# Performance work log

Hardware: AMD Instinct MI355X
Metric: run time of the kernel (lower is better)

The kernel has to match this reference:

```python
import math
import jax, jax.numpy as jnp
import numpy as np

L, B, S, D, H, F, V = 6, 2, 2048, 1024, 16, 4096, 32000
DK = D // H
EPS = 1e-5


def setup_inputs() -> dict:
    key = jax.random.key(0)
    ks = jax.random.split(key, 16)
    sc = 0.02
    inp = {
        "tokens": jax.random.randint(ks[0], (B, S), 0, V),
        "mask": jnp.ones((B, S), dtype=jnp.int32),
        "emb": jax.random.normal(ks[1], (V, D), jnp.float32) * sc,
        "Wq": jax.random.normal(ks[2], (L, D, D), jnp.float32) * sc,
        "bq": jnp.zeros((L, D), jnp.float32),
        "Wk": jax.random.normal(ks[3], (L, D, D), jnp.float32) * sc,
        "bk": jnp.zeros((L, D), jnp.float32),
        "Wv": jax.random.normal(ks[4], (L, D, D), jnp.float32) * sc,
        "bv": jnp.zeros((L, D), jnp.float32),
        "Wo": jax.random.normal(ks[5], (L, D, D), jnp.float32) * sc,
        "bo": jnp.zeros((L, D), jnp.float32),
        "W1": jax.random.normal(ks[6], (L, D, F), jnp.float32) * sc,
        "b1": jnp.zeros((L, F), jnp.float32),
        "W2": jax.random.normal(ks[7], (L, F, D), jnp.float32) * sc,
        "b2": jnp.zeros((L, D), jnp.float32),
        "g1": jnp.ones((L, D), jnp.float32),
        "be1": jnp.zeros((L, D), jnp.float32),
        "g2": jnp.ones((L, D), jnp.float32),
        "be2": jnp.zeros((L, D), jnp.float32),
        "gf": jnp.ones((D,), jnp.float32),
        "bf": jnp.zeros((D,), jnp.float32),
    }
    return inp


def _ln(x, g, b):
    m = jnp.mean(x, axis=-1, keepdims=True)
    v = jnp.var(x, axis=-1, keepdims=True)
    return (x - m) * jax.lax.rsqrt(v + EPS) * g + b


def _pos_encoding(seq_len, d_model, dtype):
    pos = jnp.arange(seq_len, dtype=jnp.float32)[:, None]
    div = jnp.exp(jnp.arange(0, d_model, 2, dtype=jnp.float32) * (-math.log(10000.0) / d_model))
    pe = jnp.zeros((seq_len, d_model), jnp.float32)
    pe = pe.at[:, 0::2].set(jnp.sin(pos * div)).at[:, 1::2].set(jnp.cos(pos * div))
    return pe.astype(dtype)


def reference(tokens, mask, emb, Wq, bq, Wk, bk, Wv, bv, Wo, bo,
              W1, b1, W2, b2, g1, be1, g2, be2, gf, bf):
    # NOTE: source scales embedding by sqrt(seq_len) (x.size(-1) of the TOKEN tensor)
    x = emb[tokens] * jnp.asarray(math.sqrt(S), emb.dtype)  # (B,S,D)
    x = x + _pos_encoding(S, D, x.dtype)[None]
    mbool = (mask == 0)[:, None, None, :]  # (B,1,1,S)
    inv_sqrt_dk = 1.0 / math.sqrt(DK)
    for i in range(L):
        h = _ln(x, g1[i], be1[i])
        q = (h @ Wq[i] + bq[i]).reshape(B, S, H, DK)
        k = (h @ Wk[i] + bk[i]).reshape(B, S, H, DK)
        v = (h @ Wv[i] + bv[i]).reshape(B, S, H, DK)
        scores = jnp.einsum('bqhd,bkhd->bhqk', q, k) * inv_sqrt_dk
        scores = jnp.where(mbool, jnp.asarray(-1e9, scores.dtype), scores)
        probs = jax.nn.softmax(scores, axis=-1)
        attn = jnp.einsum('bhqk,bkhd->bqhd', probs, v).reshape(B, S, D)
        x = x + (attn @ Wo[i] + bo[i])
        h2 = _ln(x, g2[i], be2[i])
        x = x + (jax.nn.relu(h2 @ W1[i] + b1[i]) @ W2[i] + b2[i])
    return _ln(x, gf, bf)
```

## Files before the change

### kernel.cpp

```cpp
#include <hip/hip_runtime.h>


typedef __bf16 bf16;
typedef __bf16 bf16x8 __attribute__((ext_vector_type(8)));
typedef __bf16 bf16x4 __attribute__((ext_vector_type(4)));
typedef float  f32x4  __attribute__((ext_vector_type(4)));

#define DEV __device__ __forceinline__

DEV float ld_raw(const void* p, size_t idx, int flag) {
  return flag ? (float)((const bf16*)p)[idx] : ((const float*)p)[idx];
}

DEV void gload16(const void* g, void* l) {
  __builtin_amdgcn_global_load_lds(
      (const __attribute__((address_space(1))) void*)g,
      (__attribute__((address_space(3))) void*)l, 16, 0, 0);
}

__global__ void k_sniff(const unsigned* g1, int* flag) {
  if (threadIdx.x == 0) *flag = (g1[0] == 0x3F803F80u) ? 1 : 0;
}

__global__ __launch_bounds__(256) void k_embed(
    const int* __restrict__ tokens, const void* __restrict__ emb,
    const int* __restrict__ flagp, float* __restrict__ x) {
  int row = blockIdx.x;
  int s = row & 2047;
  int flag = *flagp;
  int tok = tokens[row];
  int d0 = threadIdx.x * 4;
  float o[4];
#pragma unroll
  for (int c = 0; c < 4; ++c) {
    int d = d0 + c;
    float e = ld_raw(emb, (size_t)tok * 1024 + d, flag);
    int p2 = d & ~1;
    float div = expf((float)p2 * (-9.210340371976184f / 1024.0f));
    float arg = (float)s * div;
    float pe = (d & 1) ? cosf(arg) : sinf(arg);
    o[c] = e * 45.254833995939045f + pe;
  }
  float4 v = make_float4(o[0], o[1], o[2], o[3]);
  *(float4*)&x[(size_t)row * 1024 + d0] = v;
}

template <int OUTMODE>
__global__ __launch_bounds__(256) void k_ln(
    const float* __restrict__ x, const void* __restrict__ g,
    const void* __restrict__ b, int goff, const int* __restrict__ flagp,
    void* __restrict__ out) {
  int flag = *flagp;
  int row = blockIdx.x, t = threadIdx.x;
  float4 v = *(const float4*)&x[(size_t)row * 1024 + t * 4];
  float vv[4] = {v.x, v.y, v.z, v.w};
  float s = vv[0] + vv[1] + vv[2] + vv[3];
  float sq = vv[0]*vv[0] + vv[1]*vv[1] + vv[2]*vv[2] + vv[3]*vv[3];
#pragma unroll
  for (int off = 1; off < 64; off <<= 1) {
    s += __shfl_xor(s, off);
    sq += __shfl_xor(sq, off);
  }
  __shared__ float red[8];
  int w = t >> 6, l = t & 63;
  if (l == 0) { red[w * 2] = s; red[w * 2 + 1] = sq; }
  __syncthreads();
  s = red[0] + red[2] + red[4] + red[6];
  sq = red[1] + red[3] + red[5] + red[7];
  float mean = s * (1.0f / 1024.0f);
  float var = sq * (1.0f / 1024.0f) - mean * mean;
  float rstd = rsqrtf(var + 1e-5f);
#pragma unroll
  for (int c = 0; c < 4; ++c) {
    int d = t * 4 + c;
    float gv = ld_raw(g, (size_t)goff + d, flag);
    float bv = ld_raw(b, (size_t)goff + d, flag);
    float r = (vv[c] - mean) * rstd * gv + bv;
    size_t oi = (size_t)row * 1024 + d;
    if (OUTMODE == 0) {
      ((bf16*)out)[oi] = (bf16)r;
    } else {
      if (flag) ((unsigned short*)out)[oi] = __builtin_bit_cast(unsigned short, (bf16)r);
      else      ((float*)out)[oi] = r;
    }
  }
}

__global__ __launch_bounds__(256) void k_wtrans(
    const void* Wq, const void* Wk, const void* Wv, const void* Wo,
    const void* W1, const void* W2, int layer, const int* __restrict__ flagp,
    bf16* dQKV, bf16* dWo, bf16* dW1, bf16* dW2) {
  __shared__ bf16 tile[32][33];
  int flag = *flagp;
  int bid = blockIdx.x;
  const void* src; bf16* dst; int K, N, local; size_t soff;
  if (bid < 1024)      { src=Wq; dst=dQKV;          K=1024; N=1024; soff=(size_t)layer*1048576; local=bid; }
  else if (bid < 2048) { src=Wk; dst=dQKV+1048576;  K=1024; N=1024; soff=(size_t)layer*1048576; local=bid-1024; }
  else if (bid < 3072) { src=Wv; dst=dQKV+2097152;  K=1024; N=1024; soff=(size_t)layer*1048576; local=bid-2048; }
  else if (bid < 4096) { src=Wo; dst=dWo;           K=1024; N=1024; soff=(size_t)layer*1048576; local=bid-3072; }
  else if (bid < 8192) { src=W1; dst=dW1;           K=1024; N=4096; soff=(size_t)layer*4194304; local=bid-4096; }
  else                 { src=W2; dst=dW2;           K=4096; N=1024; soff=(size_t)layer*4194304; local=bid-8192; }
  int ntn = N >> 5;
  int k0 = (local / ntn) * 32, n0 = (local % ntn) * 32;
  int tx = threadIdx.x & 31, ty = threadIdx.x >> 5;
#pragma unroll
  for (int m = 0; m < 4; ++m) {
    int kk = k0 + ty + m * 8;
    tile[ty + m * 8][tx] = (bf16)ld_raw(src, soff + (size_t)kk * N + n0 + tx, flag);
  }
  __syncthreads();
#pragma unroll
  for (int m = 0; m < 4; ++m) {
    int nn = n0 + ty + m * 8;
    dst[(size_t)nn * K + k0 + tx] = tile[tx][ty + m * 8];
  }
}

__global__ __launch_bounds__(256) void k_vtrans(
    const bf16* __restrict__ qkv, bf16* __restrict__ Vt) {
  __shared__ bf16 tile[32][33];
  int bh = blockIdx.z, b = bh >> 4, h = bh & 15;
  int s0 = blockIdx.x * 32, d0 = blockIdx.y * 32;
  int tx = threadIdx.x & 31, ty = threadIdx.x >> 5;
#pragma unroll
  for (int m = 0; m < 4; ++m) {
    int ss = s0 + ty + m * 8;
    tile[ty + m * 8][tx] = qkv[(size_t)(b * 2048 + ss) * 3072 + 2048 + h * 64 + d0 + tx];
  }
  __syncthreads();
#pragma unroll
  for (int m = 0; m < 4; ++m) {
    int dd = d0 + ty + m * 8;
    Vt[((size_t)bh * 64 + dd) * 2048 + s0 + tx] = tile[tx][ty + m * 8];
  }
}

template <int EPI>
__global__ __launch_bounds__(256, 2) void k_gemm(
    const bf16* __restrict__ A, const bf16* __restrict__ Bt,
    void* __restrict__ Cout, int N, int K,
    const void* b0, const void* b1, const void* b2, int boff, int bseg,
    const int* __restrict__ flagp) {
  __shared__ __attribute__((aligned(16))) bf16 As[128 * 32];
  __shared__ __attribute__((aligned(16))) bf16 Bs[128 * 32];
  int flag = *flagp;
  int t = threadIdx.x, w = t >> 6, l = t & 63;
  int lr = l & 15, lh = l >> 4;
  int wr = w >> 1, wc = w & 1;
  int tm = blockIdx.y * 128, tn = blockIdx.x * 128;
  int srow = l >> 2;
  int scol = (l & 3) * 8;
  f32x4 acc[4][4] = {};
  for (int kt = 0; kt < K; kt += 32) {
    __syncthreads();
#pragma unroll
    for (int j = 0; j < 2; ++j) {
      int chunk = w * 2 + j;
      int row = chunk * 16 + srow;
      gload16(&A[(size_t)(tm + row) * K + kt + scol], &As[chunk * 512]);
      gload16(&Bt[(size_t)(tn + row) * K + kt + scol], &Bs[chunk * 512]);
    }
    __syncthreads();
    bf16x8 af[4], bfr[4];
#pragma unroll
    for (int m = 0; m < 4; ++m)
      af[m] = *(const bf16x8*)&As[(wr * 64 + m * 16 + lr) * 32 + lh * 8];
#pragma unroll
    for (int n = 0; n < 4; ++n)
      bfr[n] = *(const bf16x8*)&Bs[(wc * 64 + n * 16 + lr) * 32 + lh * 8];
#pragma unroll
    for (int m = 0; m < 4; ++m)
#pragma unroll
      for (int n = 0; n < 4; ++n)
        acc[m][n] = __builtin_amdgcn_mfma_f32_16x16x32_bf16(af[m], bfr[n], acc[m][n], 0, 0, 0);
  }
#pragma unroll
  for (int m = 0; m < 4; ++m)
#pragma unroll
    for (int n = 0; n < 4; ++n) {
      int col = tn + wc * 64 + n * 16 + lr;
      int seg = col / bseg;
      const void* bp = (seg == 0) ? b0 : ((seg == 1) ? b1 : b2);
      float bias = ld_raw(bp, (size_t)boff + (col % bseg), flag);
#pragma unroll
      for (int r = 0; r < 4; ++r) {
        int row = tm + wr * 64 + m * 16 + lh * 4 + r;
        float v = acc[m][n][r] + bias;
        size_t oi = (size_t)row * N + col;
        if (EPI == 0)      ((bf16*)Cout)[oi] = (bf16)v;
        else if (EPI == 1) ((bf16*)Cout)[oi] = (bf16)fmaxf(v, 0.0f);
        else               ((float*)Cout)[oi] += v;
      }
    }
}

__global__ __launch_bounds__(256, 2) void k_attn(
    const bf16* __restrict__ qkv, const bf16* __restrict__ Vt,
    const int* __restrict__ mask, bf16* __restrict__ out) {
  __shared__ __attribute__((aligned(16))) bf16 Ks[2][64 * 64];
  __shared__ __attribute__((aligned(16))) bf16 Vs[2][64 * 64];
  __shared__ __attribute__((aligned(16))) bf16 Ps[4][16 * 64];
  int bh = blockIdx.y, b = bh >> 4, h = bh & 15;
  int qblk = blockIdx.x;
  int t = threadIdx.x, w = t >> 6, l = t & 63, lr = l & 15, lh = l >> 4;
  int qrow = qblk * 64 + w * 16 + lr;
  int swz = (lr & 7) << 4;
  bf16x8 qf[2];
#pragma unroll
  for (int ks = 0; ks < 2; ++ks) {
    qf[ks] = *(const bf16x8*)&qkv[(size_t)(b * 2048 + qrow) * 3072 + h * 64 + ks * 32 + lh * 8];
#pragma unroll
    for (int e = 0; e < 8; ++e) qf[ks][e] = (bf16)((float)qf[ks][e] * 0.125f);
  }
  f32x4 o[4] = {};
  float mrun = -1e30f, lrun = 0.0f;
  int srow = l >> 3;
  int scb = (l & 7) * 16;
  char* PsW = (char*)&Ps[w][0];

  auto STAGE = [&](int buf, int kv0) {
#pragma unroll
    for (int j = 0; j < 2; ++j) {
      int chunk = w * 2 + j;
      int row = chunk * 8 + srow;
      int cb = scb ^ ((row & 7) << 4);
      gload16(&qkv[(size_t)(b * 2048 + kv0 + row) * 3072 + 1024 + h * 64 + (cb >> 1)], &Ks[buf][chunk * 512]);
      gload16(&Vt[((size_t)bh * 64 + row) * 2048 + kv0 + (cb >> 1)], &Vs[buf][chunk * 512]);
    }
  };

  STAGE(0, 0);
  __syncthreads();
  int cur = 0;
  for (int kv0 = 0; kv0 < 2048; kv0 += 64) {
    if (kv0 + 64 < 2048) STAGE(cur ^ 1, kv0 + 64);
    int mk = mask[b * 2048 + kv0 + l];
    const char* KsC = (const char*)&Ks[cur][0];
    const char* VsC = (const char*)&Vs[cur][0];
    f32x4 sT[4] = {};
#pragma unroll
    for (int n = 0; n < 4; ++n)
#pragma unroll
      for (int ks = 0; ks < 2; ++ks) {
        bf16x8 kf = *(const bf16x8*)(KsC + (n * 16 + lr) * 128 + ((ks * 64 + lh * 16) ^ swz));
        sT[n] = __builtin_amdgcn_mfma_f32_16x16x32_bf16(kf, qf[ks], sT[n], 0, 0, 0);
      }
    unsigned long long bal = __ballot(mk != 0);
    if (bal != 0xFFFFFFFFFFFFFFFFull) {
#pragma unroll
      for (int n = 0; n < 4; ++n)
#pragma unroll
        for (int r = 0; r < 4; ++r) {
          int ms = __shfl(mk, n * 16 + lh * 4 + r);
          if (!ms) sT[n][r] = -1e9f;
        }
    }
    float tm = sT[0][0];
#pragma unroll
    for (int n = 0; n < 4; ++n)
#pragma unroll
      for (int r = 0; r < 4; ++r) tm = fmaxf(tm, sT[n][r]);
    tm = fmaxf(tm, __shfl_xor(tm, 16));
    tm = fmaxf(tm, __shfl_xor(tm, 32));
    float mn = fmaxf(mrun, tm);
    float alpha = __expf(mrun - mn);
    mrun = mn;
    float p[4][4];
    float psum = 0.0f;
#pragma unroll
    for (int n = 0; n < 4; ++n)
#pragma unroll
      for (int r = 0; r < 4; ++r) {
        p[n][r] = __expf(sT[n][r] - mn);
        psum += p[n][r];
      }
    psum += __shfl_xor(psum, 16);
    psum += __shfl_xor(psum, 32);
    lrun = lrun * alpha + psum;
#pragma unroll
    for (int dn = 0; dn < 4; ++dn)
#pragma unroll
      for (int r = 0; r < 4; ++r) o[dn][r] *= alpha;
#pragma unroll
    for (int n = 0; n < 4; ++n) {
      bf16x4 pw = {(bf16)p[n][0], (bf16)p[n][1], (bf16)p[n][2], (bf16)p[n][3]};
      *(bf16x4*)(PsW + lr * 128 + ((n * 32 + lh * 8) ^ swz)) = pw;
    }
    bf16x8 pf[2];
#pragma unroll
    for (int ss = 0; ss < 2; ++ss)
      pf[ss] = *(const bf16x8*)(PsW + lr * 128 + ((ss * 64 + lh * 16) ^ swz));
#pragma unroll
    for (int dn = 0; dn < 4; ++dn)
#pragma unroll
      for (int ss = 0; ss < 2; ++ss) {
        bf16x8 vf = *(const bf16x8*)(VsC + (dn * 16 + lr) * 128 + ((ss * 64 + lh * 16) ^ swz));
        o[dn] = __builtin_amdgcn_mfma_f32_16x16x32_bf16(vf, pf[ss], o[dn], 0, 0, 0);
      }
    __syncthreads();
    cur ^= 1;
  }
  float inv = 1.0f / lrun;
#pragma unroll
  for (int dn = 0; dn < 4; ++dn) {
    bf16x4 ov = {(bf16)(o[dn][0] * inv), (bf16)(o[dn][1] * inv),
                 (bf16)(o[dn][2] * inv), (bf16)(o[dn][3] * inv)};
    *(bf16x4*)&out[(size_t)(b * 2048 + qrow) * 1024 + h * 64 + dn * 16 + lh * 4] = ov;
  }
}

extern "C" void kernel_launch(void* const* d_in, const int* in_sizes, int n_in,
                              void* d_out, int out_size, void* d_ws, size_t ws_size,
                              hipStream_t stream) {
  const int* tokens = (const int*)d_in[0];
  const int* maskp  = (const int*)d_in[1];
  const void* emb = d_in[2];
  const void* Wq = d_in[3];  const void* bq = d_in[4];
  const void* Wk = d_in[5];  const void* bk = d_in[6];
  const void* Wv = d_in[7];  const void* bv = d_in[8];
  const void* Wo = d_in[9];  const void* bo = d_in[10];
  const void* W1 = d_in[11]; const void* b1 = d_in[12];
  const void* W2 = d_in[13]; const void* b2 = d_in[14];
  const void* g1 = d_in[15]; const void* be1 = d_in[16];
  const void* g2 = d_in[17]; const void* be2 = d_in[18];
  const void* gf = d_in[19]; const void* bfin = d_in[20];

  char* ws = (char*)d_ws;
  int*   flag   = (int*)(ws + 0);
  float* x      = (float*)(ws + 256);
  bf16*  h      = (bf16*)(ws + 16777472);
  bf16*  qkv    = (bf16*)(ws + 25166080);
  bf16*  ff     = (bf16*)(ws + 25166080);
  bf16*  attn   = (bf16*)(ws + 50331904);
  bf16*  Vt     = (bf16*)(ws + 58720512);
  bf16*  Wqkv_t = (bf16*)(ws + 67109120);
  bf16*  Wo_t   = (bf16*)(ws + 73400576);
  bf16*  W1_t   = (bf16*)(ws + 75497728);
  bf16*  W2_t   = (bf16*)(ws + 83886336);
  if (ws_size < 92274944) return;

  k_sniff<<<1, 64, 0, stream>>>((const unsigned*)g1, flag);
  k_embed<<<4096, 256, 0, stream>>>(tokens, emb, flag, x);

  for (int i = 0; i < 6; ++i) {
    k_wtrans<<<12288, 256, 0, stream>>>(Wq, Wk, Wv, Wo, W1, W2, i, flag,
                                        Wqkv_t, Wo_t, W1_t, W2_t);
    k_ln<0><<<4096, 256, 0, stream>>>(x, g1, be1, i * 1024, flag, h);
    k_gemm<0><<<dim3(24, 32), 256, 0, stream>>>(h, Wqkv_t, qkv, 3072, 1024,
                                                bq, bk, bv, i * 1024, 1024, flag);
    k_vtrans<<<dim3(64, 2, 32), 256, 0, stream>>>(qkv, Vt);
    k_attn<<<dim3(32, 32), 256, 0, stream>>>(qkv, Vt, maskp, attn);
    k_gemm<2><<<dim3(8, 32), 256, 0, stream>>>(attn, Wo_t, x, 1024, 1024,
                                               bo, bo, bo, i * 1024, 1024, flag);
    k_ln<0><<<4096, 256, 0, stream>>>(x, g2, be2, i * 1024, flag, h);
    k_gemm<1><<<dim3(32, 32), 256, 0, stream>>>(h, W1_t, ff, 4096, 1024,
                                                b1, b1, b1, i * 4096, 4096, flag);
    k_gemm<2><<<dim3(8, 32), 256, 0, stream>>>(ff, W2_t, x, 1024, 4096,
                                               b2, b2, b2, i * 1024, 1024, flag);
  }
  k_ln<1><<<4096, 256, 0, stream>>>(x, gf, bfin, 0, flag, d_out);
}
```

Baseline: 2.276 ms.

## Double-buffer GEMM LDS, split-K residual GEMMs with atomics, remap workgroups

The GEMM kernel now double-buffers its LDS tiles, issuing the next K-slice's global-to-LDS loads before computing on the current one, and drops one barrier per iteration. The N=1024 residual GEMMs (Wo, W2) are split along K across two z-slices and accumulate into x with atomicAdd, with the bias added only by the first slice. The block-to-tile mapping is permuted in groups of 8 and launch bounds are raised to 4 waves per SIMD. This is meant to hide load latency and fill more CUs on the small-grid GEMMs, at the cost of atomic traffic, nondeterministic summation order and register pressure. The prefetch into the other buffer runs right after the end-of-iteration barrier, so it does not race with reads.

After: 2.139 ms. 6.0% less time.

```diff
diff --git a/kernel.cpp b/kernel.cpp
--- a/kernel.cpp
+++ b/kernel.cpp
@@ -136,43 +136,57 @@
 }
 
 template <int EPI>
-__global__ __launch_bounds__(256, 2) void k_gemm(
+__global__ __launch_bounds__(256, 4) void k_gemm(
     const bf16* __restrict__ A, const bf16* __restrict__ Bt,
     void* __restrict__ Cout, int N, int K,
     const void* b0, const void* b1, const void* b2, int boff, int bseg,
     const int* __restrict__ flagp) {
-  __shared__ __attribute__((aligned(16))) bf16 As[128 * 32];
-  __shared__ __attribute__((aligned(16))) bf16 Bs[128 * 32];
+  __shared__ __attribute__((aligned(16))) bf16 As[2][128 * 32];
+  __shared__ __attribute__((aligned(16))) bf16 Bs[2][128 * 32];
   int flag = *flagp;
   int t = threadIdx.x, w = t >> 6, l = t & 63;
   int lr = l & 15, lh = l >> 4;
   int wr = w >> 1, wc = w & 1;
-  int tm = blockIdx.y * 128, tn = blockIdx.x * 128;
+  int gx = gridDim.x;
+  int nwg = gx * gridDim.y;
+  int bid = blockIdx.y * gx + blockIdx.x;
+  int wid = (nwg & 7) ? bid : ((bid & 7) * (nwg >> 3) + (bid >> 3));
+  int tm = (wid / gx) * 128, tn = (wid % gx) * 128;
+  int Kc = K / gridDim.z;
+  int kbeg = blockIdx.z * Kc, kend = kbeg + Kc;
   int srow = l >> 2;
   int scol = (l & 3) * 8;
   f32x4 acc[4][4] = {};
-  for (int kt = 0; kt < K; kt += 32) {
-    __syncthreads();
+
+  auto STAGE = [&](int buf, int kt) {
 #pragma unroll
     for (int j = 0; j < 2; ++j) {
       int chunk = w * 2 + j;
       int row = chunk * 16 + srow;
-      gload16(&A[(size_t)(tm + row) * K + kt + scol], &As[chunk * 512]);
-      gload16(&Bt[(size_t)(tn + row) * K + kt + scol], &Bs[chunk * 512]);
-    }
-    __syncthreads();
+      gload16(&A[(size_t)(tm + row) * K + kt + scol], &As[buf][chunk * 512]);
+      gload16(&Bt[(size_t)(tn + row) * K + kt + scol], &Bs[buf][chunk * 512]);
+    }
+  };
+
+  STAGE(0, kbeg);
+  __syncthreads();
+  int cur = 0;
+  for (int kt = kbeg; kt < kend; kt += 32) {
+    if (kt + 32 < kend) STAGE(cur ^ 1, kt + 32);
     bf16x8 af[4], bfr[4];
 #pragma unroll
     for (int m = 0; m < 4; ++m)
-      af[m] = *(const bf16x8*)&As[(wr * 64 + m * 16 + lr) * 32 + lh * 8];
+      af[m] = *(const bf16x8*)&As[cur][(wr * 64 + m * 16 + lr) * 32 + lh * 8];
 #pragma unroll
     for (int n = 0; n < 4; ++n)
-      bfr[n] = *(const bf16x8*)&Bs[(wc * 64 + n * 16 + lr) * 32 + lh * 8];
+      bfr[n] = *(const bf16x8*)&Bs[cur][(wc * 64 + n * 16 + lr) * 32 + lh * 8];
 #pragma unroll
     for (int m = 0; m < 4; ++m)
 #pragma unroll
       for (int n = 0; n < 4; ++n)
         acc[m][n] = __builtin_amdgcn_mfma_f32_16x16x32_bf16(af[m], bfr[n], acc[m][n], 0, 0, 0);
+    __syncthreads();
+    cur ^= 1;
   }
 #pragma unroll
   for (int m = 0; m < 4; ++m)
@@ -181,7 +195,7 @@
       int col = tn + wc * 64 + n * 16 + lr;
       int seg = col / bseg;
       const void* bp = (seg == 0) ? b0 : ((seg == 1) ? b1 : b2);
-      float bias = ld_raw(bp, (size_t)boff + (col % bseg), flag);
+      float bias = (blockIdx.z == 0) ? ld_raw(bp, (size_t)boff + (col % bseg), flag) : 0.0f;
 #pragma unroll
       for (int r = 0; r < 4; ++r) {
         int row = tm + wr * 64 + m * 16 + lh * 4 + r;
@@ -189,7 +203,7 @@
         size_t oi = (size_t)row * N + col;
         if (EPI == 0)      ((bf16*)Cout)[oi] = (bf16)v;
         else if (EPI == 1) ((bf16*)Cout)[oi] = (bf16)fmaxf(v, 0.0f);
-        else               ((float*)Cout)[oi] += v;
+        else               atomicAdd(&((float*)Cout)[oi], v);
       }
     }
 }
@@ -350,13 +364,13 @@
                                                 bq, bk, bv, i * 1024, 1024, flag);
     k_vtrans<<<dim3(64, 2, 32), 256, 0, stream>>>(qkv, Vt);
     k_attn<<<dim3(32, 32), 256, 0, stream>>>(qkv, Vt, maskp, attn);
-    k_gemm<2><<<dim3(8, 32), 256, 0, stream>>>(attn, Wo_t, x, 1024, 1024,
-                                               bo, bo, bo, i * 1024, 1024, flag);
+    k_gemm<2><<<dim3(8, 32, 2), 256, 0, stream>>>(attn, Wo_t, x, 1024, 1024,
+                                                  bo, bo, bo, i * 1024, 1024, flag);
     k_ln<0><<<4096, 256, 0, stream>>>(x, g2, be2, i * 1024, flag, h);
     k_gemm<1><<<dim3(32, 32), 256, 0, stream>>>(h, W1_t, ff, 4096, 1024,
                                                 b1, b1, b1, i * 4096, 4096, flag);
-    k_gemm<2><<<dim3(8, 32), 256, 0, stream>>>(ff, W2_t, x, 1024, 4096,
-                                               b2, b2, b2, i * 1024, 1024, flag);
+    k_gemm<2><<<dim3(8, 32, 2), 256, 0, stream>>>(ff, W2_t, x, 1024, 4096,
+                                                  b2, b2, b2, i * 1024, 1024, flag);
   }
   k_ln<1><<<4096, 256, 0, stream>>>(x, gf, bfin, 0, flag, d_out);
 }
```
